# Performance work log

Hardware: AMD Instinct MI355X
Metric: run time of the kernel (lower is better)

## Reference

```python
import jax, jax.numpy as jnp
import numpy as np

BATCH = 16384
NUM_FEATURES = 1024  # sum(field_dims)
CROSS_DIMS = NUM_FEATURES * (NUM_FEATURES - 1) // 2  # 523776


def setup_inputs() -> dict:
    key = jax.random.key(0)
    kx, kw = jax.random.split(key)
    x = jax.random.uniform(kx, (BATCH, NUM_FEATURES), dtype=jnp.float32)
    # xavier-uniform init of a (cross_dims, 1) parameter: bound = sqrt(6/(fan_in+fan_out))
    bound = float(np.sqrt(6.0 / (CROSS_DIMS + 1)))
    w = jax.random.uniform(kw, (CROSS_DIMS,), dtype=jnp.float32, minval=-bound, maxval=bound)
    return {"x": x, "w": w}


def reference(x, w):
    # POLY2: out_b = sigmoid( sum_{i<j} w_{ij} * x_{b,i} * x_{b,j} )
    # sklearn PolynomialFeatures(interaction_only) emits pairs in combinations
    # (row-major i<j) order, identical to triu_indices(k=1) ordering.
    F = x.shape[1]
    iu, ju = jnp.triu_indices(F, k=1)
    W = jnp.zeros((F, F), dtype=x.dtype).at[iu, ju].set(w)  # [F,F] strictly upper-tri
    # quadratic form without materializing the [B, F*(F-1)/2] pairwise matrix
    out = jnp.einsum('bi,ij,bj->b', x, W, x)  # [B]
    return jax.nn.sigmoid(out.astype(jnp.float32))
```

## Files before the change

### kernel.cpp

```cpp
#include <hip/hip_runtime.h>
#include <hip/hip_bf16.h>

#define F 1024
#define B_ROWS 16384

typedef short v8s __attribute__((ext_vector_type(8)));
typedef float v4f __attribute__((ext_vector_type(4)));
typedef unsigned short v8u __attribute__((ext_vector_type(8)));
typedef unsigned short ushort_t;

__device__ __forceinline__ unsigned short f2bf(float f) {
    unsigned int u = __builtin_bit_cast(unsigned int, f);
    u = (u + 0x7FFFu + ((u >> 16) & 1u)) >> 16;
    return (unsigned short)u;
}

__device__ __forceinline__ void gload_lds16(const ushort_t* g, ushort_t* l) {
    __builtin_amdgcn_global_load_lds(
        (const __attribute__((address_space(1))) unsigned int*)g,
        (__attribute__((address_space(3))) unsigned int*)l,
        16, 0, 0);
}


__global__ __launch_bounds__(256) void prep_kernel(
        const float* __restrict__ w, const float* __restrict__ x,
        ushort_t* __restrict__ Bp, ushort_t* __restrict__ Xp,
        float* __restrict__ acc) {
    const int bid  = blockIdx.x;
    const int tid  = threadIdx.x;
    const int lane = tid & 63;
    const int wave = tid >> 6;
    const int l16  = lane & 15;
    const int quad = lane >> 4;

    if (bid < 64) {
        acc[bid * 256 + tid] = 0.0f;
    } else if (bid < 576) {
        const int c  = (bid - 64) * 4 + wave;
        const int n  = (c >> 5) * 16 + l16;
        const int k0 = (c & 31) * 32 + quad * 8;
        v8u o;
#pragma unroll
        for (int e = 0; e < 8; ++e) {
            const int k = k0 + e;
            float v = 0.0f;
            if (k < n) {
                const int idx = k * (F - 1) - (k * (k - 1)) / 2 + (n - k - 1);
                v = w[idx];
            }
            o[e] = f2bf(v);
        }
        *(v8u*)(Bp + (size_t)c * 512 + lane * 8) = o;
    } else {
        const int c  = (bid - 576) * 4 + wave;
        const int r  = (c >> 5) * 16 + l16;
        const int k0 = (c & 31) * 32 + quad * 8;
        const float* src = x + (size_t)r * F + k0;
        float4 v0 = *(const float4*)(src);
        float4 v1 = *(const float4*)(src + 4);
        v8u o;
        o[0] = f2bf(v0.x); o[1] = f2bf(v0.y); o[2] = f2bf(v0.z); o[3] = f2bf(v0.w);
        o[4] = f2bf(v1.x); o[5] = f2bf(v1.y); o[6] = f2bf(v1.z); o[7] = f2bf(v1.w);
        *(v8u*)(Xp + (size_t)c * 512 + lane * 8) = o;
    }
}

__global__ __launch_bounds__(256, 4) void gemm_kernel(
        const ushort_t* __restrict__ Xp,
        const ushort_t* __restrict__ Bp,
        const float*   __restrict__ Xf,
        float*         __restrict__ rowacc) {
    __shared__ ushort_t Ls[2 * 16 * 512];

    const int f   = blockIdx.x;
    const int xcd = f & 7;
    const int g   = f >> 3;
    const int y   = g & 15;
    const int nt  = 7 - (g >> 4);
    const int blockM = (xcd * 16 + y) * 128;
    const int blockN = nt * 128;
    const int tEnd   = 4 * (nt + 1);

    const int tid   = threadIdx.x;
    const int lane  = tid & 63;
    const int wave  = tid >> 6;
    const int waveM = wave >> 1;
    const int waveN = wave & 1;
    const int quad  = lane >> 4;
    const int l16   = lane & 15;

    const int mgBase = blockM >> 4;
    const int ngB    = nt * 8;

    const bool stageA = (wave < 2);
    const int  qBase  = (wave & 1) * 4;
    const ushort_t* gsrc0 = stageA
        ? Xp + ((size_t)(mgBase + qBase) * 32) * 512
        : Bp + ((size_t)(ngB  + qBase) * 32) * 512;
    const int slot0 = (stageA ? 0 : 8) + qBase;

#define STAGE(t, buf)                                                          \
    {                                                                          \
        _Pragma("unroll")                                                      \
        for (int q = 0; q < 4; ++q) {                                          \
            gload_lds16(gsrc0 + ((size_t)q * 32 + (t)) * 512 + lane * 8,       \
                        Ls + ((buf) * 16 + slot0 + q) * 512);                  \
        }                                                                      \
    }

    v4f acc[4][4];
#pragma unroll
    for (int i = 0; i < 4; i++)
#pragma unroll
        for (int j = 0; j < 4; j++) acc[i][j] = (v4f)(0.0f);

    v8s afr[4], bfr[4];

    STAGE(0, 0)
    __syncthreads();

    for (int t = 0; t < tEnd; ++t) {
        const int  buf  = t & 1;
        const bool more = (t + 1 < tEnd);
        if (more) STAGE(t + 1, buf ^ 1)

#pragma unroll
        for (int mi = 0; mi < 4; ++mi)
            afr[mi] = *(const v8s*)(Ls + (buf * 16 + waveM * 4 + mi) * 512 + lane * 8);
#pragma unroll
        for (int ni = 0; ni < 4; ++ni)
            bfr[ni] = *(const v8s*)(Ls + (buf * 16 + 8 + waveN * 4 + ni) * 512 + lane * 8);

#pragma unroll
        for (int mi = 0; mi < 4; ++mi)
#pragma unroll
            for (int ni = 0; ni < 4; ++ni)
                acc[mi][ni] = __builtin_amdgcn_mfma_f32_16x16x32_bf16(
                    afr[mi], bfr[ni], acc[mi][ni], 0, 0, 0);

        if (more) __syncthreads();
    }
#undef STAGE

#pragma unroll
    for (int mi = 0; mi < 4; mi++) {
#pragma unroll
        for (int r = 0; r < 4; r++) {
            const int b = blockM + waveM * 64 + mi * 16 + quad * 4 + r;
            const float* xr = Xf + (size_t)b * F + blockN + waveN * 64 + l16;
            float pv = acc[mi][0][r] * xr[0]
                     + acc[mi][1][r] * xr[16]
                     + acc[mi][2][r] * xr[32]
                     + acc[mi][3][r] * xr[48];
            pv += __shfl_xor(pv, 1);
            pv += __shfl_xor(pv, 2);
            pv += __shfl_xor(pv, 4);
            pv += __shfl_xor(pv, 8);
            if (l16 == 0) atomicAdd(&rowacc[b], pv);
        }
    }
}

__global__ void sigmoid_kernel(const float* __restrict__ acc, float* __restrict__ out) {
    int b = blockIdx.x * blockDim.x + threadIdx.x;
    out[b] = 1.0f / (1.0f + __expf(-acc[b]));
}

__global__ void fallback_kernel(const float* __restrict__ x, const float* __restrict__ w,
                                float* __restrict__ out) {
    __shared__ float xs[F];
    __shared__ float partial[4];
    const int b = blockIdx.x;
    for (int i = threadIdx.x; i < F; i += 256) xs[i] = x[(size_t)b * F + i];
    __syncthreads();
    float s = 0.0f;
    for (int i = threadIdx.x; i < F - 1; i += 256) {
        const float xi = xs[i];
        const int kbase = i * (F - 1) - (i * (i - 1)) / 2 - i - 1;
        for (int j = i + 1; j < F; j++) s += w[kbase + j] * xi * xs[j];
    }
    for (int off = 32; off; off >>= 1) s += __shfl_down(s, off);
    if ((threadIdx.x & 63) == 0) partial[threadIdx.x >> 6] = s;
    __syncthreads();
    if (threadIdx.x == 0) {
        float t = partial[0] + partial[1] + partial[2] + partial[3];
        out[b] = 1.0f / (1.0f + __expf(-t));
    }
}

extern "C" void kernel_launch(void* const* d_in, const int* in_sizes, int n_in,
                              void* d_out, int out_size, void* d_ws, size_t ws_size,
                              hipStream_t stream) {
    const float* x = (const float*)d_in[0];
    const float* w = (const float*)d_in[1];
    float* out = (float*)d_out;

    const size_t acc_bytes = 65536;
    const size_t B_bytes   = (size_t)F * F * 2;
    const size_t Xp_bytes  = (size_t)B_ROWS * F * 2;
    const size_t needed = acc_bytes + B_bytes + Xp_bytes;

    if (ws_size < needed) {
        fallback_kernel<<<B_ROWS, 256, 0, stream>>>(x, w, out);
        return;
    }

    float*    acc = (float*)d_ws;
    ushort_t* Bp  = (ushort_t*)((char*)d_ws + acc_bytes);
    ushort_t* Xp  = (ushort_t*)((char*)d_ws + acc_bytes + B_bytes);

    prep_kernel<<<64 + 512 + 8192, 256, 0, stream>>>(w, x, Bp, Xp, acc);
    gemm_kernel<<<1024, 256, 0, stream>>>(Xp, Bp, x, acc);
    sigmoid_kernel<<<B_ROWS / 256, 256, 0, stream>>>(acc, out);
}
```

Before: 128.2 us.

## Enlarge GEMM tiles to 256x256 with 512 threads and split-K triangular job balancing

The triangular GEMM moves from 128x128 tiles with 256 threads to 256x256 tiles with 8 waves. Each wave accumulates an 8x4 grid of MFMA tiles and stages 64 KB per buffer in dynamic LDS, 128 KB in total. The upper-triangular work is cut into equal-size split-K jobs from a constant table, so each of the 512 blocks gets a balanced chunk instead of the earlier per-nt variable-length loops. The aim is higher arithmetic intensity and better load balance. The cost is much more register and LDS pressure, which likely allows only one block per CU, and more atomics per row.

```diff
diff --git a/kernel.cpp b/kernel.cpp
--- a/kernel.cpp
+++ b/kernel.cpp
@@ -66,89 +66,99 @@
     }
 }
 
-__global__ __launch_bounds__(256, 4) void gemm_kernel(
+__device__ __constant__ int JOB_NT[2][4] = {{2, 2, 3, 3}, {0, 1, 1, 3}};
+__device__ __constant__ int JOB_C0[2][4] = {{0, 6, 0, 6}, {0, 0, 4, 12}};
+__device__ __constant__ int JOB_NC[2][4] = {{6, 6, 6, 6}, {4, 4, 4, 4}};
+
+__global__ __launch_bounds__(512, 2) void gemm_kernel(
         const ushort_t* __restrict__ Xp,
         const ushort_t* __restrict__ Bp,
         const float*   __restrict__ Xf,
         float*         __restrict__ rowacc) {
-    __shared__ ushort_t Ls[2 * 16 * 512];
-
-    const int f   = blockIdx.x;
-    const int xcd = f & 7;
-    const int g   = f >> 3;
-    const int y   = g & 15;
-    const int nt  = 7 - (g >> 4);
-    const int blockM = (xcd * 16 + y) * 128;
-    const int blockN = nt * 128;
-    const int tEnd   = 4 * (nt + 1);
+    extern __shared__ ushort_t Ls[];
+
+    const int b  = blockIdx.x;
+    const int h  = b >> 8;
+    const int j  = b & 3;
+    const int mt = (b >> 2) & 63;
+    const int NT = JOB_NT[h][j];
+    const int c0 = JOB_C0[h][j];
+    const int nc = JOB_NC[h][j];
+    const int blockM = mt * 256;
+    const int blockN = NT * 256;
+    const int tEnd   = c0 + nc;
 
     const int tid   = threadIdx.x;
     const int lane  = tid & 63;
     const int wave  = tid >> 6;
-    const int waveM = wave >> 1;
-    const int waveN = wave & 1;
+    const int waveM = wave >> 2;
+    const int waveN = wave & 3;
     const int quad  = lane >> 4;
     const int l16   = lane & 15;
 
-    const int mgBase = blockM >> 4;
-    const int ngB    = nt * 8;
-
-    const bool stageA = (wave < 2);
-    const int  qBase  = (wave & 1) * 4;
-    const ushort_t* gsrc0 = stageA
-        ? Xp + ((size_t)(mgBase + qBase) * 32) * 512
-        : Bp + ((size_t)(ngB  + qBase) * 32) * 512;
-    const int slot0 = (stageA ? 0 : 8) + qBase;
+    const int q0 = wave * 8;
 
 #define STAGE(t, buf)                                                          \
     {                                                                          \
         _Pragma("unroll")                                                      \
-        for (int q = 0; q < 4; ++q) {                                          \
-            gload_lds16(gsrc0 + ((size_t)q * 32 + (t)) * 512 + lane * 8,       \
-                        Ls + ((buf) * 16 + slot0 + q) * 512);                  \
+        for (int q = 0; q < 8; ++q) {                                          \
+            const int qq = q0 + q;                                             \
+            const ushort_t* src;                                               \
+            if (qq < 32) {                                                     \
+                src = Xp + ((size_t)(mt * 16 + (qq >> 1)) * 32                 \
+                            + 2 * (t) + (qq & 1)) * 512 + lane * 8;            \
+            } else {                                                           \
+                src = Bp + ((size_t)(NT * 16 + ((qq - 32) >> 1)) * 32          \
+                            + 2 * (t) + (qq & 1)) * 512 + lane * 8;            \
+            }                                                                  \
+            gload_lds16(src, Ls + ((buf) * 64 + qq) * 512);                    \
         }                                                                      \
     }
 
-    v4f acc[4][4];
-#pragma unroll
-    for (int i = 0; i < 4; i++)
-#pragma unroll
-        for (int j = 0; j < 4; j++) acc[i][j] = (v4f)(0.0f);
-
-    v8s afr[4], bfr[4];
-
-    STAGE(0, 0)
+    v4f acc[8][4];
+#pragma unroll
+    for (int i = 0; i < 8; i++)
+#pragma unroll
+        for (int jj = 0; jj < 4; jj++) acc[i][jj] = (v4f)(0.0f);
+
+    v8s afr[8], bfr[4];
+
+    STAGE(c0, 0)
     __syncthreads();
 
-    for (int t = 0; t < tEnd; ++t) {
-        const int  buf  = t & 1;
+    for (int t = c0; t < tEnd; ++t) {
+        const int  buf  = (t - c0) & 1;
         const bool more = (t + 1 < tEnd);
         if (more) STAGE(t + 1, buf ^ 1)
 
 #pragma unroll
-        for (int mi = 0; mi < 4; ++mi)
-            afr[mi] = *(const v8s*)(Ls + (buf * 16 + waveM * 4 + mi) * 512 + lane * 8);
-#pragma unroll
-        for (int ni = 0; ni < 4; ++ni)
-            bfr[ni] = *(const v8s*)(Ls + (buf * 16 + 8 + waveN * 4 + ni) * 512 + lane * 8);
-
-#pragma unroll
-        for (int mi = 0; mi < 4; ++mi)
+        for (int kg = 0; kg < 2; ++kg) {
+#pragma unroll
+            for (int mi = 0; mi < 8; ++mi)
+                afr[mi] = *(const v8s*)(Ls + ((buf * 64)
+                           + (waveM * 8 + mi) * 2 + kg) * 512 + lane * 8);
 #pragma unroll
             for (int ni = 0; ni < 4; ++ni)
-                acc[mi][ni] = __builtin_amdgcn_mfma_f32_16x16x32_bf16(
-                    afr[mi], bfr[ni], acc[mi][ni], 0, 0, 0);
+                bfr[ni] = *(const v8s*)(Ls + ((buf * 64) + 32
+                           + (waveN * 4 + ni) * 2 + kg) * 512 + lane * 8);
+#pragma unroll
+            for (int mi = 0; mi < 8; ++mi)
+#pragma unroll
+                for (int ni = 0; ni < 4; ++ni)
+                    acc[mi][ni] = __builtin_amdgcn_mfma_f32_16x16x32_bf16(
+                        afr[mi], bfr[ni], acc[mi][ni], 0, 0, 0);
+        }
 
         if (more) __syncthreads();
     }
 #undef STAGE
 
 #pragma unroll
-    for (int mi = 0; mi < 4; mi++) {
+    for (int mi = 0; mi < 8; mi++) {
 #pragma unroll
         for (int r = 0; r < 4; r++) {
-            const int b = blockM + waveM * 64 + mi * 16 + quad * 4 + r;
-            const float* xr = Xf + (size_t)b * F + blockN + waveN * 64 + l16;
+            const int bb = blockM + waveM * 128 + mi * 16 + quad * 4 + r;
+            const float* xr = Xf + (size_t)bb * F + blockN + waveN * 64 + l16;
             float pv = acc[mi][0][r] * xr[0]
                      + acc[mi][1][r] * xr[16]
                      + acc[mi][2][r] * xr[32]
@@ -157,7 +167,7 @@
             pv += __shfl_xor(pv, 2);
             pv += __shfl_xor(pv, 4);
             pv += __shfl_xor(pv, 8);
-            if (l16 == 0) atomicAdd(&rowacc[b], pv);
+            if (l16 == 0) atomicAdd(&rowacc[bb], pv);
         }
     }
 }
@@ -206,11 +216,18 @@
         return;
     }
 
+    static bool lds_inited = false;
+    if (!lds_inited) {
+        hipFuncSetAttribute((const void*)gemm_kernel,
+                            hipFuncAttributeMaxDynamicSharedMemorySize, 131072);
+        lds_inited = true;
+    }
+
     float*    acc = (float*)d_ws;
     ushort_t* Bp  = (ushort_t*)((char*)d_ws + acc_bytes);
     ushort_t* Xp  = (ushort_t*)((char*)d_ws + acc_bytes + B_bytes);
 
     prep_kernel<<<64 + 512 + 8192, 256, 0, stream>>>(w, x, Bp, Xp, acc);
-    gemm_kernel<<<1024, 256, 0, stream>>>(Xp, Bp, x, acc);
+    gemm_kernel<<<512, 512, 131072, stream>>>(Xp, Bp, x, acc);
     sigmoid_kernel<<<B_ROWS / 256, 256, 0, stream>>>(acc, out);
 }
```

Result: slower. 151.7 us (+18.4%).
